# Performance work log

Hardware: AMD Instinct MI355X
Metric: run time of the kernel (lower is better)

## Reference

```python
import jax, jax.numpy as jnp
import numpy as np

B, S, D = 2, 2048, 768
C = 8                # num_channels
R = D // C           # ternary_rank = 96 (RoPE head_dim)
THETA = 10000.0
TERNARY_STD = 0.2
TERNARY_SCALE = 1.0  # ternary_factor_scaling


def _rope_tables():
    # HF-style RoPE: inv_freq over half dim, emb = concat(freqs, freqs)
    inv_freq = 1.0 / (THETA ** (np.arange(0, R, 2, dtype=np.float32) / R))
    pos = np.arange(S, dtype=np.float32)
    freqs = pos[:, None] * inv_freq[None, :]          # [S, R/2]
    emb = np.concatenate([freqs, freqs], axis=-1)     # [S, R]
    cos = np.broadcast_to(np.cos(emb)[None], (B, S, R)).copy()
    sin = np.broadcast_to(np.sin(emb)[None], (B, S, R)).copy()
    return jnp.asarray(cos), jnp.asarray(sin)


def setup_inputs() -> dict:
    key = jax.random.key(0)
    k1, k2, k3 = jax.random.split(key, 3)
    qz = jax.random.normal(k1, (B, S, D), dtype=jnp.float32)
    U = jax.random.normal(k2, (D, D), dtype=jnp.float32) * TERNARY_STD
    V = jax.random.normal(k3, (D, D), dtype=jnp.float32) * TERNARY_STD
    cos, sin = _rope_tables()
    return {"qz": qz, "cos": cos, "sin": sin, "U": U, "V": V}


def _rotate_half(x):
    h = x.shape[-1] // 2
    return jnp.concatenate([-x[..., h:], x[..., :h]], axis=-1)


def reference(qz, cos, sin, U, V):
    # cos/sin: [B,S,R] -> broadcast over channel dim -> [B,1,S,R]
    cosb = cos[:, None, :, :]
    sinb = sin[:, None, :, :]
    rope = lambda x: x * cosb + _rotate_half(x) * sinb       # apply
    rope_o = lambda x: x * cosb - _rotate_half(x) * sinb     # apply_o (inverse)

    # projections: F.linear(qz, W) == qz @ W.T
    qz_u = (qz @ U.T * TERNARY_SCALE).reshape(B, S, C, R).transpose(0, 2, 1, 3)
    qz_v = (qz @ V.T * TERNARY_SCALE).reshape(B, S, C, R).transpose(0, 2, 1, 3)

    qz_uo = rope_o(qz_u)
    qz_ur = rope(qz_u)
    qz_vr = rope(qz_v)

    # message_F: [B,C,S,S]
    message_F = jnp.einsum('bcqr,bckr->bcqk', qz_ur, qz_vr)
    # softmax(message_F / regularize_h) with regularize_h = 1/D  ->  * D
    qh = jax.nn.softmax((message_F * jnp.float32(D)).astype(jnp.float32), axis=-1).astype(qz_ur.dtype)

    qh_v1 = rope_o(jnp.einsum('bcqk,bckr->bcqr', qh, qz_vr))  # qh @ qz_v
    qh_v2 = rope(jnp.einsum('bckq,bckr->bcqr', qh, qz_uo))    # qh^T @ qz_uo

    qh_v1 = qh_v1.transpose(0, 2, 1, 3).reshape(B, S, D)
    qh_v2 = qh_v2.transpose(0, 2, 1, 3).reshape(B, S, D)

    message_G = (qh_v1 @ U + qh_v2 @ V) * TERNARY_SCALE
    return message_G
```

## Files before the change

kernel.cpp:

```cpp
#include <hip/hip_runtime.h>

typedef _Float16 f16;
typedef _Float16 f16x8 __attribute__((ext_vector_type(8)));
typedef _Float16 f16x4 __attribute__((ext_vector_type(4)));
typedef float f32x4 __attribute__((ext_vector_type(4)));

#define MFMA16(A,B,C) __builtin_amdgcn_mfma_f32_16x16x32_f16(A,B,C,0,0,0)
#define INV2048 4.8828125e-4f
#define HN (16ll*2048*96)
#define UVN 589824
#define ZC1 1107.98979f
#define ZC2 0.54101064f

__device__ __forceinline__ void split_f16(float x, f16& h, f16& l) {
    h = (f16)x;
    l = (f16)((x - (float)h) * 2048.0f);
}

__global__ __launch_bounds__(256) void k0_split(const float* __restrict__ qz,
                                                const float* __restrict__ U,
                                                const float* __restrict__ V,
                                                f16* __restrict__ qzh, f16* __restrict__ qzl,
                                                f16* __restrict__ Uh, f16* __restrict__ Ul,
                                                f16* __restrict__ Vh, f16* __restrict__ Vl) {
    const int i4 = blockIdx.x * 256 + threadIdx.x;
    {
        float4 x = *(const float4*)(qz + (size_t)i4 * 4);
        f16 h0, l0, h1, l1, h2, l2, h3, l3;
        split_f16(x.x, h0, l0); split_f16(x.y, h1, l1);
        split_f16(x.z, h2, l2); split_f16(x.w, h3, l3);
        f16x4 hv = {h0, h1, h2, h3};
        f16x4 lv = {l0, l1, l2, l3};
        *(f16x4*)(qzh + (size_t)i4 * 4) = hv;
        *(f16x4*)(qzl + (size_t)i4 * 4) = lv;
    }
    if (i4 < UVN / 4) {
        float4 x = *(const float4*)(U + (size_t)i4 * 4);
        f16 h0, l0, h1, l1, h2, l2, h3, l3;
        split_f16(x.x, h0, l0); split_f16(x.y, h1, l1);
        split_f16(x.z, h2, l2); split_f16(x.w, h3, l3);
        f16x4 hv = {h0, h1, h2, h3};
        f16x4 lv = {l0, l1, l2, l3};
        *(f16x4*)(Uh + (size_t)i4 * 4) = hv;
        *(f16x4*)(Ul + (size_t)i4 * 4) = lv;
        float4 y = *(const float4*)(V + (size_t)i4 * 4);
        split_f16(y.x, h0, l0); split_f16(y.y, h1, l1);
        split_f16(y.z, h2, l2); split_f16(y.w, h3, l3);
        f16x4 hv2 = {h0, h1, h2, h3};
        f16x4 lv2 = {l0, l1, l2, l3};
        *(f16x4*)(Vh + (size_t)i4 * 4) = hv2;
        *(f16x4*)(Vl + (size_t)i4 * 4) = lv2;
    }
}

__global__ __launch_bounds__(256, 2) void k1_proj(const f16* __restrict__ qzh,
                                                  const f16* __restrict__ qzl,
                                                  const f16* __restrict__ Uh,
                                                  const f16* __restrict__ Ul,
                                                  const f16* __restrict__ Vh,
                                                  const f16* __restrict__ Vl,
                                                  const float* __restrict__ cosb,
                                                  const float* __restrict__ sinb,
                                                  f16* __restrict__ uhp, f16* __restrict__ ulp,
                                                  f16* __restrict__ vhp, f16* __restrict__ vlp,
                                                  f16* __restrict__ vT, f16* __restrict__ oT) {
    __shared__ __align__(16) f16 smem[36864];
    f16* sAh  = smem;
    f16* sAl  = smem + 4608;
    f16* sBuh = smem + 9216;
    f16* sBul = smem + 9216 + 6912;
    f16* sBvh = smem + 9216 + 2 * 6912;
    f16* sBvl = smem + 9216 + 3 * 6912;

    const int tid = threadIdx.x;
    const int w = tid >> 6, lane = tid & 63;
    const int quad = lane >> 4, l15 = lane & 15;
    const int wr = w >> 1, wc = w & 1;
    const int bs0 = blockIdx.x * 64;
    const int c = blockIdx.y;

    const f16* Ug_h = Uh + (size_t)c * 96 * 768;
    const f16* Ug_l = Ul + (size_t)c * 96 * 768;
    const f16* Vg_h = Vh + (size_t)c * 96 * 768;
    const f16* Vg_l = Vl + (size_t)c * 96 * 768;

    f32x4 aUS[2][3] = {}, aUX[2][3] = {};
    f32x4 aVS[2][3] = {}, aVX[2][3] = {};

    for (int k0 = 0; k0 < 768; k0 += 64) {
        __syncthreads();
#pragma unroll
        for (int m = 0; m < 2; ++m) {
            int f = tid + 256 * m, row = f >> 3, cg = f & 7;
            const size_t go = (size_t)(bs0 + row) * 768 + k0 + cg * 8;
            const int lo = row * 72 + cg * 8;
            *(float4*)&sAh[lo] = *(const float4*)(qzh + go);
            *(float4*)&sAl[lo] = *(const float4*)(qzl + go);
        }
#pragma unroll
        for (int m = 0; m < 3; ++m) {
            int f = tid + 256 * m, row = f >> 3, cg = f & 7;
            const size_t go = (size_t)row * 768 + k0 + cg * 8;
            const int lo = row * 72 + cg * 8;
            *(float4*)&sBuh[lo] = *(const float4*)(Ug_h + go);
            *(float4*)&sBul[lo] = *(const float4*)(Ug_l + go);
            *(float4*)&sBvh[lo] = *(const float4*)(Vg_h + go);
            *(float4*)&sBvl[lo] = *(const float4*)(Vg_l + go);
        }
        __syncthreads();
#pragma unroll
        for (int cc = 0; cc < 2; ++cc) {
            f16x8 ah[2], al[2];
#pragma unroll
            for (int mt = 0; mt < 2; ++mt) {
                const int ar = (32 * wr + 16 * mt + l15) * 72 + cc * 32 + quad * 8;
                ah[mt] = *(const f16x8*)&sAh[ar];
                al[mt] = *(const f16x8*)&sAl[ar];
            }
#pragma unroll
            for (int nt = 0; nt < 3; ++nt) {
                const int br = (48 * wc + 16 * nt + l15) * 72 + cc * 32 + quad * 8;
                f16x8 buh = *(const f16x8*)&sBuh[br];
                f16x8 bul = *(const f16x8*)&sBul[br];
                f16x8 bvh = *(const f16x8*)&sBvh[br];
                f16x8 bvl = *(const f16x8*)&sBvl[br];
#pragma unroll
                for (int mt = 0; mt < 2; ++mt) {
                    aUS[mt][nt] = MFMA16(ah[mt], buh, aUS[mt][nt]);
                    aUX[mt][nt] = MFMA16(ah[mt], bul, aUX[mt][nt]);
                    aUX[mt][nt] = MFMA16(al[mt], buh, aUX[mt][nt]);
                    aVS[mt][nt] = MFMA16(ah[mt], bvh, aVS[mt][nt]);
                    aVX[mt][nt] = MFMA16(ah[mt], bvl, aVX[mt][nt]);
// ... 15 lines not shown
                const int sl = 32 * wr + 16 * mt + 4 * quad + r;
                const int col = 48 * wc + 16 * nt + l15;
                LU[sl * 100 + col] = aUS[mt][nt][r] + aUX[mt][nt][r] * INV2048;
                LV[sl * 100 + col] = aVS[mt][nt][r] + aVX[mt][nt][r] * INV2048;
            }
    __syncthreads();

    const int b = bs0 >> 11;
    const int s0 = bs0 & 2047;
    const int head = b * 8 + c;
    const size_t nb = (size_t)head * 2048 * 96;
    const size_t tb = (size_t)head * 96 * 2048;
    const int ty = tid >> 4, tx = tid & 15;

#pragma unroll
    for (int jj = 0; jj < 3; ++jj) {
        int r = tx + 16 * jj;
        f16 vt1[4], vt2[4], ot1[4], ot2[4];
#pragma unroll
        for (int ii = 0; ii < 4; ++ii) {
            int sl = 4 * ty + ii;
            int s = s0 + sl;
            int cbi = (b * 2048 + s) * 96 + r;
            float cc = cosb[cbi], ss = sinb[cbi];
            size_t rowb = nb + (size_t)s * 96;
            float u1 = LU[sl * 100 + r], u2 = LU[sl * 100 + r + 48];
            float v1 = LV[sl * 100 + r], v2 = LV[sl * 100 + r + 48];
            float ur1 = u1 * cc - u2 * ss, ur2 = u2 * cc + u1 * ss;
            float uo1 = u1 * cc + u2 * ss, uo2 = u2 * cc - u1 * ss;
            float vr1 = v1 * cc - v2 * ss, vr2 = v2 * cc + v1 * ss;
            f16 h, l;
            split_f16(ur1, h, l); uhp[rowb + r] = h;      ulp[rowb + r] = l;
            split_f16(ur2, h, l); uhp[rowb + r + 48] = h; ulp[rowb + r + 48] = l;
            split_f16(vr1, h, l); vhp[rowb + r] = h;      vlp[rowb + r] = l;      vt1[ii] = h;
            split_f16(vr2, h, l); vhp[rowb + r + 48] = h; vlp[rowb + r + 48] = l; vt2[ii] = h;
            ot1[ii] = (f16)uo1; ot2[ii] = (f16)uo2;
        }
        f16x4 pv1 = {vt1[0], vt1[1], vt1[2], vt1[3]};
        f16x4 pv2 = {vt2[0], vt2[1], vt2[2], vt2[3]};
        f16x4 po1 = {ot1[0], ot1[1], ot1[2], ot1[3]};
        f16x4 po2 = {ot2[0], ot2[1], ot2[2], ot2[3]};
        *(f16x4*)&vT[tb + (size_t)r * 2048 + s0 + 4 * ty] = pv1;
        *(f16x4*)&vT[tb + (size_t)(r + 48) * 2048 + s0 + 4 * ty] = pv2;
        *(f16x4*)&oT[tb + (size_t)r * 2048 + s0 + 4 * ty] = po1;
        *(f16x4*)&oT[tb + (size_t)(r + 48) * 2048 + s0 + 4 * ty] = po2;
    }
}

__global__ __launch_bounds__(256, 2) void k2_stats(const f16* __restrict__ uhp,
                                                   const f16* __restrict__ ulp,
                                                   const f16* __restrict__ vhp,
                                                   const f16* __restrict__ vlp,
                                                   float* __restrict__ Mo) {
    __shared__ f16 Bh[64 * 104];
    __shared__ f16 Bl[64 * 104];
    __shared__ float Mbuf[4][64];
    const int tid = threadIdx.x, w = tid >> 6, lane = tid & 63;
    const int quad = lane >> 4, l15 = lane & 15;
    const int q0 = blockIdx.x * 64, head = blockIdx.y;
    const f16* Ah_g = uhp + (size_t)head * 2048 * 96;
    const f16* Al_g = ulp + (size_t)head * 2048 * 96;
    const f16* Bh_g = vhp + (size_t)head * 2048 * 96;
    const f16* Bl_g = vlp + (size_t)head * 2048 * 96;

    f16x8 Afh[4][3], Afl[4][3];
#pragma unroll
    for (int mt = 0; mt < 4; ++mt)
#pragma unroll
        for (int cc = 0; cc < 3; ++cc) {
            size_t off = (size_t)(q0 + 16 * mt + l15) * 96 + cc * 32 + quad * 8;
            Afh[mt][cc] = *(const f16x8*)(Ah_g + off);
            Afl[mt][cc] = *(const f16x8*)(Al_g + off);
        }

    float m_run[4][4];
#pragma unroll
    for (int mt = 0; mt < 4; ++mt)
#pragma unroll
        for (int r = 0; r < 4; ++r) m_run[mt][r] = -3.0e38f;

    for (int k0 = 0; k0 < 2048; k0 += 64) {
        __syncthreads();
#pragma unroll
        for (int m = 0; m < 3; ++m) {
            int f = tid + 256 * m;
            int row = f / 12, c12 = f % 12;
            *(float4*)&Bh[row * 104 + c12 * 8] =
                *(const float4*)(Bh_g + (size_t)(k0 + row) * 96 + c12 * 8);
            *(float4*)&Bl[row * 104 + c12 * 8] =
                *(const float4*)(Bl_g + (size_t)(k0 + row) * 96 + c12 * 8);
        }
        __syncthreads();
        f32x4 accS[4] = {}, accX[4] = {};
#pragma unroll
        for (int cc = 0; cc < 3; ++cc) {
            f16x8 bh = *(const f16x8*)&Bh[(w * 16 + l15) * 104 + cc * 32 + quad * 8];
            f16x8 bl = *(const f16x8*)&Bl[(w * 16 + l15) * 104 + cc * 32 + quad * 8];
#pragma unroll
            for (int mt = 0; mt < 4; ++mt) {
                accS[mt] = MFMA16(Afh[mt][cc], bh, accS[mt]);
                accX[mt] = MFMA16(Afh[mt][cc], bl, accX[mt]);
                accX[mt] = MFMA16(Afl[mt][cc], bh, accX[mt]);
            }
        }
#pragma unroll
        for (int mt = 0; mt < 4; ++mt)
#pragma unroll
            for (int r = 0; r < 4; ++r) {
                float zl = fmaf(ZC1, accS[mt][r], ZC2 * accX[mt][r]);
                m_run[mt][r] = fmaxf(m_run[mt][r], zl);
            }
    }
#pragma unroll
    for (int mt = 0; mt < 4; ++mt)
#pragma unroll
        for (int r = 0; r < 4; ++r) {
            float m = m_run[mt][r];
            m = fmaxf(m, __shfl_xor(m, 1)); m = fmaxf(m, __shfl_xor(m, 2));
            m = fmaxf(m, __shfl_xor(m, 4)); m = fmaxf(m, __shfl_xor(m, 8));
            m_run[mt][r] = m;
        }
    if (l15 == 0) {
#pragma unroll
        for (int mt = 0; mt < 4; ++mt)
#pragma unroll
            for (int r = 0; r < 4; ++r)
                Mbuf[w][16 * mt + 4 * quad + r] = m_run[mt][r];
    }
    __syncthreads();
    if (tid < 64) {
        float M = -3.0e38f;
#pragma unroll
        for (int ww = 0; ww < 4; ++ww) M = fmaxf(M, Mbuf[ww][tid]);
        Mo[head * 2048 + q0 + tid] = M;
    }
}

__global__ __launch_bounds__(256, 2) void k3a(const f16* __restrict__ uhp,
                                              const f16* __restrict__ ulp,
                                              const f16* __restrict__ vhp,
                                              const f16* __restrict__ vlp,
                                              const f16* __restrict__ vT,
                                              const float* __restrict__ Mo,
                                              float* __restrict__ Lo,
                                              const float* __restrict__ cosb,
                                              const float* __restrict__ sinb,
                                              f16* __restrict__ w1) {
    __shared__ f16 Bh[64 * 104];
    __shared__ f16 Bl[64 * 104];
    __shared__ f16 Vt[112 * 72];
    __shared__ f16 P[64 * 72];
    const int tid = threadIdx.x, w = tid >> 6, lane = tid & 63;
    const int quad = lane >> 4, l15 = lane & 15;
    const int q0 = blockIdx.x * 64, head = blockIdx.y;
    const f16* Ah_g = uhp + (size_t)head * 2048 * 96;
    const f16* Al_g = ulp + (size_t)head * 2048 * 96;
    const f16* Bh_g = vhp + (size_t)head * 2048 * 96;
    const f16* Bl_g = vlp + (size_t)head * 2048 * 96;
    const f16* Vt_g = vT + (size_t)head * 96 * 2048;

    f16x8 Afh[4][3], Afl[4][3];
#pragma unroll
    for (int mt = 0; mt < 4; ++mt)
#pragma unroll
        for (int cc = 0; cc < 3; ++cc) {
            size_t off = (size_t)(q0 + 16 * mt + l15) * 96 + cc * 32 + quad * 8;
            Afh[mt][cc] = *(const f16x8*)(Ah_g + off);
            Afl[mt][cc] = *(const f16x8*)(Al_g + off);
        }
    float negM[4][4];
#pragma unroll
    for (int mt = 0; mt < 4; ++mt)
#pragma unroll
        for (int r = 0; r < 4; ++r)
            negM[mt][r] = -Mo[head * 2048 + q0 + 16 * mt + 4 * quad + r];

    if (tid < 144) {
        f16x8 ones = {(f16)1, (f16)1, (f16)1, (f16)1,
                      (f16)1, (f16)1, (f16)1, (f16)1};
        *(f16x8*)&Vt[96 * 72 + tid * 8] = ones;
    }

    f32x4 accO[7] = {};

    for (int k0 = 0; k0 < 2048; k0 += 64) {
        __syncthreads();
#pragma unroll
        for (int m = 0; m < 3; ++m) {
            int f = tid + 256 * m;
            int row = f / 12, c12 = f % 12;
            *(float4*)&Bh[row * 104 + c12 * 8] =
                *(const float4*)(Bh_g + (size_t)(k0 + row) * 96 + c12 * 8);
            *(float4*)&Bl[row * 104 + c12 * 8] =
                *(const float4*)(Bl_g + (size_t)(k0 + row) * 96 + c12 * 8);
        }
#pragma unroll
        for (int m = 0; m < 3; ++m) {
            int f = tid + 256 * m;
            int row = f >> 3, c8 = f & 7;
            *(float4*)&Vt[row * 72 + c8 * 8] =
                *(const float4*)(Vt_g + (size_t)row * 2048 + k0 + c8 * 8);
        }
        __syncthreads();
        f32x4 accS[4] = {}, accX[4] = {};
#pragma unroll
        for (int cc = 0; cc < 3; ++cc) {
            f16x8 bh = *(const f16x8*)&Bh[(w * 16 + l15) * 104 + cc * 32 + quad * 8];
            f16x8 bl = *(const f16x8*)&Bl[(w * 16 + l15) * 104 + cc * 32 + quad * 8];
#pragma unroll
            for (int mt = 0; mt < 4; ++mt) {
                accS[mt] = MFMA16(Afh[mt][cc], bh, accS[mt]);
                accX[mt] = MFMA16(Afh[mt][cc], bl, accX[mt]);
                accX[mt] = MFMA16(Afl[mt][cc], bh, accX[mt]);
            }
        }
#pragma unroll
        for (int mt = 0; mt < 4; ++mt)
#pragma unroll
            for (int r = 0; r < 4; ++r) {
                float zl = fmaf(ZC1, accS[mt][r], ZC2 * accX[mt][r]);
                P[(16 * mt + 4 * quad + r) * 72 + w * 16 + l15] =
                    (f16)exp2f(zl + negM[mt][r]);
            }
        __syncthreads();
#pragma unroll
        for (int kc = 0; kc < 2; ++kc) {
            f16x8 ap = *(const f16x8*)&P[(w * 16 + l15) * 72 + kc * 32 + quad * 8];
#pragma unroll
            for (int nt = 0; nt < 7; ++nt) {
                f16x8 bv = *(const f16x8*)&Vt[(nt * 16 + l15) * 72 + kc * 32 + quad * 8];
                accO[nt] = MFMA16(ap, bv, accO[nt]);
            }
        }
        __syncthreads();
    }
    float invL[4];
#pragma unroll
    for (int r = 0; r < 4; ++r) invL[r] = 1.0f / accO[6][r];
    if (l15 == 0) {
#pragma unroll
        for (int r = 0; r < 4; ++r)
            Lo[head * 2048 + q0 + w * 16 + quad * 4 + r] = accO[6][r];
    }

    const int b = head >> 3, c = head & 7;
#pragma unroll
    for (int r = 0; r < 4; ++r) {
        int q = q0 + w * 16 + quad * 4 + r;
        int cbi = (b * 2048 + q) * 96;
        f16* wrow = w1 + (size_t)(b * 2048 + q) * 768 + c * 96;
#pragma unroll
        for (int nt = 0; nt < 3; ++nt) {
            int rr = nt * 16 + l15;
            float cc = cosb[cbi + rr], ss = sinb[cbi + rr];
            float a = accO[nt][r] * invL[r];
            float b2 = accO[nt + 3][r] * invL[r];
            wrow[rr] = (f16)(a * cc + b2 * ss);
            wrow[rr + 48] = (f16)(b2 * cc - a * ss);
        }
    }
}

__global__ __launch_bounds__(256, 2) void k3b(const f16* __restrict__ uhp,
                                              const f16* __restrict__ ulp,
                                              const f16* __restrict__ vhp,
                                              const f16* __restrict__ vlp,
                                              const f16* __restrict__ oT,
                                              const float* __restrict__ Mo,
                                              const float* __restrict__ Lo,
                                              const float* __restrict__ cosb,
                                              const float* __restrict__ sinb,
                                              f16* __restrict__ w2) {
    __shared__ f16 Bh[64 * 104];
    __shared__ f16 Bl[64 * 104];
    __shared__ f16 Ot[96 * 72];
    __shared__ f16 P[64 * 72];
    const int tid = threadIdx.x, w = tid >> 6, lane = tid & 63;
    const int quad = lane >> 4, l15 = lane & 15;
    const int q0 = blockIdx.x * 64, head = blockIdx.y;
    const f16* Ah_g = vhp + (size_t)head * 2048 * 96;
    const f16* Al_g = vlp + (size_t)head * 2048 * 96;
    const f16* Bh_g = uhp + (size_t)head * 2048 * 96;
    const f16* Bl_g = ulp + (size_t)head * 2048 * 96;
    const f16* Ot_g = oT + (size_t)head * 96 * 2048;

    f16x8 Afh[4][3], Afl[4][3];
#pragma unroll
    for (int mt = 0; mt < 4; ++mt)
#pragma unroll
        for (int cc = 0; cc < 3; ++cc) {
            size_t off = (size_t)(q0 + 16 * mt + l15) * 96 + cc * 32 + quad * 8;
            Afh[mt][cc] = *(const f16x8*)(Ah_g + off);
            Afl[mt][cc] = *(const f16x8*)(Al_g + off);
        }

    f32x4 accO[6] = {};

    for (int k0 = 0; k0 < 2048; k0 += 64) {
        float negMk = -Mo[head * 2048 + k0 + w * 16 + l15];
        float invLk = 1.0f / Lo[head * 2048 + k0 + w * 16 + l15];
        __syncthreads();
#pragma unroll
        for (int m = 0; m < 3; ++m) {
            int f = tid + 256 * m;
            int row = f / 12, c12 = f % 12;
            *(float4*)&Bh[row * 104 + c12 * 8] =
                *(const float4*)(Bh_g + (size_t)(k0 + row) * 96 + c12 * 8);
            *(float4*)&Bl[row * 104 + c12 * 8] =
                *(const float4*)(Bl_g + (size_t)(k0 + row) * 96 + c12 * 8);
        }
#pragma unroll
        for (int m = 0; m < 3; ++m) {
            int f = tid + 256 * m;
            int row = f >> 3, c8 = f & 7;
            *(float4*)&Ot[row * 72 + c8 * 8] =
                *(const float4*)(Ot_g + (size_t)row * 2048 + k0 + c8 * 8);
        }
        __syncthreads();
        f32x4 accS[4] = {}, accX[4] = {};
#pragma unroll
        for (int cc = 0; cc < 3; ++cc) {
            f16x8 bh = *(const f16x8*)&Bh[(w * 16 + l15) * 104 + cc * 32 + quad * 8];
            f16x8 bl = *(const f16x8*)&Bl[(w * 16 + l15) * 104 + cc * 32 + quad * 8];
#pragma unroll
            for (int mt = 0; mt < 4; ++mt) {
                accS[mt] = MFMA16(Afh[mt][cc], bh, accS[mt]);
                accX[mt] = MFMA16(Afl[mt][cc], bh, accX[mt]);
                accX[mt] = MFMA16(Afh[mt][cc], bl, accX[mt]);
            }
        }
#pragma unroll
        for (int mt = 0; mt < 4; ++mt)
#pragma unroll
            for (int r = 0; r < 4; ++r) {
                float zl = fmaf(ZC1, accS[mt][r], ZC2 * accX[mt][r]);
                P[(16 * mt + 4 * quad + r) * 72 + w * 16 + l15] =
                    (f16)(exp2f(zl + negMk) * invLk);
            }
        __syncthreads();
#pragma unroll
        for (int kc = 0; kc < 2; ++kc) {
            f16x8 ap = *(const f16x8*)&P[(w * 16 + l15) * 72 + kc * 32 + quad * 8];
#pragma unroll
            for (int nt = 0; nt < 6; ++nt) {
                f16x8 bo = *(const f16x8*)&Ot[(nt * 16 + l15) * 72 + kc * 32 + quad * 8];
                accO[nt] = MFMA16(ap, bo, accO[nt]);
            }
        }
        __syncthreads();
    }
    const int b = head >> 3, c = head & 7;
#pragma unroll
    for (int r = 0; r < 4; ++r) {
        int q = q0 + w * 16 + quad * 4 + r;
        int cbi = (b * 2048 + q) * 96;
        f16* wrow = w2 + (size_t)(b * 2048 + q) * 768 + c * 96;
#pragma unroll
        for (int nt = 0; nt < 3; ++nt) {
            int rr = nt * 16 + l15;
            float cc = cosb[cbi + rr], ss = sinb[cbi + rr];
            float a = accO[nt][r];
            float b2 = accO[nt + 3][r];
            wrow[rr] = (f16)(a * cc - b2 * ss);
            wrow[rr + 48] = (f16)(b2 * cc + a * ss);
        }
    }
}

__global__ __launch_bounds__(256, 2) void k4_final(const f16* __restrict__ w1,
                                                   const f16* __restrict__ w2,
                                                   const float* __restrict__ U,
                                                   const float* __restrict__ V,
                                                   float* __restrict__ outp) {
    __shared__ f16 A1[128 * 56];
    __shared__ f16 A2[128 * 56];
    __shared__ f16 B1[64 * 56];
    __shared__ f16 B2[64 * 56];
    const int tid = threadIdx.x, w = tid >> 6, lane = tid & 63;
    const int quad = lane >> 4, l15 = lane & 15;
    const int bs0 = blockIdx.x * 128;
    const int d0 = blockIdx.y * 64;
    f32x4 acc[2][4] = {};

    for (int ec = 0; ec < 24; ++ec) {
        int e0 = ec * 32;
        __syncthreads();
#pragma unroll
        for (int m = 0; m < 2; ++m) {
            int f = tid + 256 * m;
            int row = f >> 2, q = f & 3;
            *(float4*)&A1[row * 56 + q * 8] =
                *(const float4*)(w1 + (size_t)(bs0 + row) * 768 + e0 + q * 8);
            *(float4*)&A2[row * 56 + q * 8] =
                *(const float4*)(w2 + (size_t)(bs0 + row) * 768 + e0 + q * 8);
        }
#pragma unroll
        for (int m2 = 0; m2 < 2; ++m2) {
            int e_r = (tid >> 4) + 16 * m2;
            int dc = tid & 15;
            float4 fu = *(const float4*)(U + (size_t)(e0 + e_r) * 768 + d0 + dc * 4);
            float4 fv = *(const float4*)(V + (size_t)(e0 + e_r) * 768 + d0 + dc * 4);
            B1[(dc * 4 + 0) * 56 + e_r] = (f16)fu.x;
// ... 77 lines not shown
```

Measured before the change: 339.8 us.

## Prefetch next K tile into registers and double-buffer shared tiles in attention kernels

The stats, k3a and k3b kernels now issue global loads for the next 64-row K/V tile into registers before computing on the current tile, then write them to shared memory after the score MFMAs. Vt/Ot (and Bh/Bl in k2_stats) are double-buffered so the store does not race with readers, and one barrier per iteration is removed in k2. This aims to hide global load latency behind MFMA work, at the cost of extra LDS and registers, which may reduce occupancy under launch_bounds(256,2).

```diff
diff --git a/kernel.cpp b/kernel.cpp
--- a/kernel.cpp
+++ b/kernel.cpp
@@ -199,8 +199,8 @@
                                                    const f16* __restrict__ vhp,
                                                    const f16* __restrict__ vlp,
                                                    float* __restrict__ Mo) {
-    __shared__ f16 Bh[64 * 104];
-    __shared__ f16 Bl[64 * 104];
+    __shared__ f16 Bh[2][64 * 104];
+    __shared__ f16 Bl[2][64 * 104];
     __shared__ float Mbuf[4][64];
     const int tid = threadIdx.x, w = tid >> 6, lane = tid & 63;
     const int quad = lane >> 4, l15 = lane & 15;
@@ -220,29 +220,49 @@
             Afl[mt][cc] = *(const f16x8*)(Al_g + off);
         }
 
+    const int sr0 = tid / 12,         sc0 = (tid % 12) * 8;
+    const int sr1 = (tid + 256) / 12, sc1 = ((tid + 256) % 12) * 8;
+    const int sr2 = (tid + 512) / 12, sc2 = ((tid + 512) % 12) * 8;
+
+    float4 h0, h1, h2, g0, g1, g2;
+
     float m_run[4][4];
 #pragma unroll
     for (int mt = 0; mt < 4; ++mt)
 #pragma unroll
         for (int r = 0; r < 4; ++r) m_run[mt][r] = -3.0e38f;
 
-    for (int k0 = 0; k0 < 2048; k0 += 64) {
-        __syncthreads();
-#pragma unroll
-        for (int m = 0; m < 3; ++m) {
-            int f = tid + 256 * m;
-            int row = f / 12, c12 = f % 12;
-            *(float4*)&Bh[row * 104 + c12 * 8] =
-                *(const float4*)(Bh_g + (size_t)(k0 + row) * 96 + c12 * 8);
-            *(float4*)&Bl[row * 104 + c12 * 8] =
-                *(const float4*)(Bl_g + (size_t)(k0 + row) * 96 + c12 * 8);
-        }
-        __syncthreads();
+    h0 = *(const float4*)(Bh_g + (size_t)sr0 * 96 + sc0);
+    h1 = *(const float4*)(Bh_g + (size_t)sr1 * 96 + sc1);
+    h2 = *(const float4*)(Bh_g + (size_t)sr2 * 96 + sc2);
+    g0 = *(const float4*)(Bl_g + (size_t)sr0 * 96 + sc0);
+    g1 = *(const float4*)(Bl_g + (size_t)sr1 * 96 + sc1);
+    g2 = *(const float4*)(Bl_g + (size_t)sr2 * 96 + sc2);
+    *(float4*)&Bh[0][sr0 * 104 + sc0] = h0;
+    *(float4*)&Bh[0][sr1 * 104 + sc1] = h1;
+    *(float4*)&Bh[0][sr2 * 104 + sc2] = h2;
+    *(float4*)&Bl[0][sr0 * 104 + sc0] = g0;
+    *(float4*)&Bl[0][sr1 * 104 + sc1] = g1;
+    *(float4*)&Bl[0][sr2 * 104 + sc2] = g2;
+    __syncthreads();
+
+    for (int t = 0; t < 32; ++t) {
+        const int cur = t & 1;
+        if (t < 31) {
+            const f16* bg = Bh_g + (size_t)(t + 1) * 6144;
+            const f16* lg = Bl_g + (size_t)(t + 1) * 6144;
+            h0 = *(const float4*)(bg + (size_t)sr0 * 96 + sc0);
+            h1 = *(const float4*)(bg + (size_t)sr1 * 96 + sc1);
+            h2 = *(const float4*)(bg + (size_t)sr2 * 96 + sc2);
+            g0 = *(const float4*)(lg + (size_t)sr0 * 96 + sc0);
+            g1 = *(const float4*)(lg + (size_t)sr1 * 96 + sc1);
+            g2 = *(const float4*)(lg + (size_t)sr2 * 96 + sc2);
+        }
         f32x4 accS[4] = {}, accX[4] = {};
 #pragma unroll
         for (int cc = 0; cc < 3; ++cc) {
-            f16x8 bh = *(const f16x8*)&Bh[(w * 16 + l15) * 104 + cc * 32 + quad * 8];
-            f16x8 bl = *(const f16x8*)&Bl[(w * 16 + l15) * 104 + cc * 32 + quad * 8];
+            f16x8 bh = *(const f16x8*)&Bh[cur][(w * 16 + l15) * 104 + cc * 32 + quad * 8];
+            f16x8 bl = *(const f16x8*)&Bl[cur][(w * 16 + l15) * 104 + cc * 32 + quad * 8];
 #pragma unroll
             for (int mt = 0; mt < 4; ++mt) {
                 accS[mt] = MFMA16(Afh[mt][cc], bh, accS[mt]);
@@ -257,6 +277,15 @@
                 float zl = fmaf(ZC1, accS[mt][r], ZC2 * accX[mt][r]);
                 m_run[mt][r] = fmaxf(m_run[mt][r], zl);
             }
+        if (t < 31) {
+            *(float4*)&Bh[cur ^ 1][sr0 * 104 + sc0] = h0;
+            *(float4*)&Bh[cur ^ 1][sr1 * 104 + sc1] = h1;
+            *(float4*)&Bh[cur ^ 1][sr2 * 104 + sc2] = h2;
+            *(float4*)&Bl[cur ^ 1][sr0 * 104 + sc0] = g0;
+            *(float4*)&Bl[cur ^ 1][sr1 * 104 + sc1] = g1;
+            *(float4*)&Bl[cur ^ 1][sr2 * 104 + sc2] = g2;
+        }
+        __syncthreads();
     }
 #pragma unroll
     for (int mt = 0; mt < 4; ++mt)
@@ -295,7 +324,7 @@
                                               f16* __restrict__ w1) {
     __shared__ f16 Bh[64 * 104];
     __shared__ f16 Bl[64 * 104];
-    __shared__ f16 Vt[112 * 72];
+    __shared__ f16 Vt[2][112 * 72];
     __shared__ f16 P[64 * 72];
     const int tid = threadIdx.x, w = tid >> 6, lane = tid & 63;
     const int quad = lane >> 4, l15 = lane & 15;
@@ -322,33 +351,58 @@
         for (int r = 0; r < 4; ++r)
             negM[mt][r] = -Mo[head * 2048 + q0 + 16 * mt + 4 * quad + r];
 
+    const int sr0 = tid / 12,         sc0 = (tid % 12) * 8;
+    const int sr1 = (tid + 256) / 12, sc1 = ((tid + 256) % 12) * 8;
+    const int sr2 = (tid + 512) / 12, sc2 = ((tid + 512) % 12) * 8;
+    const int vr0 = tid >> 3, vcc = (tid & 7) * 8;
+
+    float4 h0, h1, h2, g0, g1, g2, v0, v1, v2;
+
     if (tid < 144) {
         f16x8 ones = {(f16)1, (f16)1, (f16)1, (f16)1,
                       (f16)1, (f16)1, (f16)1, (f16)1};
-        *(f16x8*)&Vt[96 * 72 + tid * 8] = ones;
-    }
+        *(f16x8*)&Vt[0][96 * 72 + tid * 8] = ones;
+        *(f16x8*)&Vt[1][96 * 72 + tid * 8] = ones;
+    }
+
+    h0 = *(const float4*)(Bh_g + (size_t)sr0 * 96 + sc0);
+    h1 = *(const float4*)(Bh_g + (size_t)sr1 * 96 + sc1);
+    h2 = *(const float4*)(Bh_g + (size_t)sr2 * 96 + sc2);
+    g0 = *(const float4*)(Bl_g + (size_t)sr0 * 96 + sc0);
+    g1 = *(const float4*)(Bl_g + (size_t)sr1 * 96 + sc1);
+    g2 = *(const float4*)(Bl_g + (size_t)sr2 * 96 + sc2);
+    v0 = *(const float4*)(Vt_g + (size_t)vr0 * 2048 + vcc);
+    v1 = *(const float4*)(Vt_g + (size_t)(vr0 + 32) * 2048 + vcc);
+    v2 = *(const float4*)(Vt_g + (size_t)(vr0 + 64) * 2048 + vcc);
+    *(float4*)&Bh[sr0 * 104 + sc0] = h0;
+    *(float4*)&Bh[sr1 * 104 + sc1] = h1;
+    *(float4*)&Bh[sr2 * 104 + sc2] = h2;
+    *(float4*)&Bl[sr0 * 104 + sc0] = g0;
+    *(float4*)&Bl[sr1 * 104 + sc1] = g1;
+    *(float4*)&Bl[sr2 * 104 + sc2] = g2;
+    *(float4*)&Vt[0][vr0 * 72 + vcc] = v0;
+    *(float4*)&Vt[0][(vr0 + 32) * 72 + vcc] = v1;
+    *(float4*)&Vt[0][(vr0 + 64) * 72 + vcc] = v2;
+    __syncthreads();
 
     f32x4 accO[7] = {};
-
-    for (int k0 = 0; k0 < 2048; k0 += 64) {
-        __syncthreads();
-#pragma unroll
-        for (int m = 0; m < 3; ++m) {
-            int f = tid + 256 * m;
-            int row = f / 12, c12 = f % 12;
-            *(float4*)&Bh[row * 104 + c12 * 8] =
-                *(const float4*)(Bh_g + (size_t)(k0 + row) * 96 + c12 * 8);
-            *(float4*)&Bl[row * 104 + c12 * 8] =
-                *(const float4*)(Bl_g + (size_t)(k0 + row) * 96 + c12 * 8);
-        }
-#pragma unroll
-        for (int m = 0; m < 3; ++m) {
-            int f = tid + 256 * m;
-            int row = f >> 3, c8 = f & 7;
-            *(float4*)&Vt[row * 72 + c8 * 8] =
-                *(const float4*)(Vt_g + (size_t)row * 2048 + k0 + c8 * 8);
-        }
-        __syncthreads();
+    int pcur = 0;
+
+    for (int t = 0; t < 32; ++t) {
+        if (t < 31) {
+            const f16* bg = Bh_g + (size_t)(t + 1) * 6144;
+            const f16* lg = Bl_g + (size_t)(t + 1) * 6144;
+            const int kn = (t + 1) * 64;
+            h0 = *(const float4*)(bg + (size_t)sr0 * 96 + sc0);
+            h1 = *(const float4*)(bg + (size_t)sr1 * 96 + sc1);
+            h2 = *(const float4*)(bg + (size_t)sr2 * 96 + sc2);
+            g0 = *(const float4*)(lg + (size_t)sr0 * 96 + sc0);
+            g1 = *(const float4*)(lg + (size_t)sr1 * 96 + sc1);
+            g2 = *(const float4*)(lg + (size_t)sr2 * 96 + sc2);
+            v0 = *(const float4*)(Vt_g + (size_t)vr0 * 2048 + kn + vcc);
+            v1 = *(const float4*)(Vt_g + (size_t)(vr0 + 32) * 2048 + kn + vcc);
+            v2 = *(const float4*)(Vt_g + (size_t)(vr0 + 64) * 2048 + kn + vcc);
+        }
         f32x4 accS[4] = {}, accX[4] = {};
 #pragma unroll
         for (int cc = 0; cc < 3; ++cc) {
@@ -370,16 +424,28 @@
                     (f16)exp2f(zl + negM[mt][r]);
             }
         __syncthreads();
+        if (t < 31) {
+            *(float4*)&Bh[sr0 * 104 + sc0] = h0;
+            *(float4*)&Bh[sr1 * 104 + sc1] = h1;
+            *(float4*)&Bh[sr2 * 104 + sc2] = h2;
+            *(float4*)&Bl[sr0 * 104 + sc0] = g0;
+            *(float4*)&Bl[sr1 * 104 + sc1] = g1;
+            *(float4*)&Bl[sr2 * 104 + sc2] = g2;
+            *(float4*)&Vt[pcur ^ 1][vr0 * 72 + vcc] = v0;
+            *(float4*)&Vt[pcur ^ 1][(vr0 + 32) * 72 + vcc] = v1;
+            *(float4*)&Vt[pcur ^ 1][(vr0 + 64) * 72 + vcc] = v2;
+        }
 #pragma unroll
         for (int kc = 0; kc < 2; ++kc) {
             f16x8 ap = *(const f16x8*)&P[(w * 16 + l15) * 72 + kc * 32 + quad * 8];
 #pragma unroll
             for (int nt = 0; nt < 7; ++nt) {
-                f16x8 bv = *(const f16x8*)&Vt[(nt * 16 + l15) * 72 + kc * 32 + quad * 8];
+                f16x8 bv = *(const f16x8*)&Vt[pcur][(nt * 16 + l15) * 72 + kc * 32 + quad * 8];
                 accO[nt] = MFMA16(ap, bv, accO[nt]);
             }
         }
         __syncthreads();
+        pcur ^= 1;
     }
     float invL[4];
 #pragma unroll
@@ -420,7 +486,7 @@
                                               f16* __restrict__ w2) {
     __shared__ f16 Bh[64 * 104];
     __shared__ f16 Bl[64 * 104];
-    __shared__ f16 Ot[96 * 72];
+    __shared__ f16 Ot[2][96 * 72];
     __shared__ f16 P[64 * 72];
     const int tid = threadIdx.x, w = tid >> 6, lane = tid & 63;
     const int quad = lane >> 4, l15 = lane & 15;
@@ -441,29 +507,54 @@
             Afl[mt][cc] = *(const f16x8*)(Al_g + off);
         }
 
+    const int sr0 = tid / 12,         sc0 = (tid % 12) * 8;
+    const int sr1 = (tid + 256) / 12, sc1 = ((tid + 256) % 12) * 8;
+    const int sr2 = (tid + 512) / 12, sc2 = ((tid + 512) % 12) * 8;
+    const int vr0 = tid >> 3, vcc = (tid & 7) * 8;
+
+    float4 h0, h1, h2, g0, g1, g2, v0, v1, v2;
+
+    h0 = *(const float4*)(Bh_g + (size_t)sr0 * 96 + sc0);
+    h1 = *(const float4*)(Bh_g + (size_t)sr1 * 96 + sc1);
+    h2 = *(const float4*)(Bh_g + (size_t)sr2 * 96 + sc2);
+    g0 = *(const float4*)(Bl_g + (size_t)sr0 * 96 + sc0);
+    g1 = *(const float4*)(Bl_g + (size_t)sr1 * 96 + sc1);
+    g2 = *(const float4*)(Bl_g + (size_t)sr2 * 96 + sc2);
+    v0 = *(const float4*)(Ot_g + (size_t)vr0 * 2048 + vcc);
+    v1 = *(const float4*)(Ot_g + (size_t)(vr0 + 32) * 2048 + vcc);
+    v2 = *(const float4*)(Ot_g + (size_t)(vr0 + 64) * 2048 + vcc);
+    *(float4*)&Bh[sr0 * 104 + sc0] = h0;
+    *(float4*)&Bh[sr1 * 104 + sc1] = h1;
+    *(float4*)&Bh[sr2 * 104 + sc2] = h2;
+    *(float4*)&Bl[sr0 * 104 + sc0] = g0;
+    *(float4*)&Bl[sr1 * 104 + sc1] = g1;
+    *(float4*)&Bl[sr2 * 104 + sc2] = g2;
+    *(float4*)&Ot[0][vr0 * 72 + vcc] = v0;
+    *(float4*)&Ot[0][(vr0 + 32) * 72 + vcc] = v1;
+    *(float4*)&Ot[0][(vr0 + 64) * 72 + vcc] = v2;
+    __syncthreads();
+
     f32x4 accO[6] = {};
-
-    for (int k0 = 0; k0 < 2048; k0 += 64) {
+    int pcur = 0;
+
+    for (int t = 0; t < 32; ++t) {
+        const int k0 = t * 64;
         float negMk = -Mo[head * 2048 + k0 + w * 16 + l15];
         float invLk = 1.0f / Lo[head * 2048 + k0 + w * 16 + l15];
-        __syncthreads();
-#pragma unroll
-        for (int m = 0; m < 3; ++m) {
-            int f = tid + 256 * m;
-            int row = f / 12, c12 = f % 12;
-            *(float4*)&Bh[row * 104 + c12 * 8] =
-                *(const float4*)(Bh_g + (size_t)(k0 + row) * 96 + c12 * 8);
-            *(float4*)&Bl[row * 104 + c12 * 8] =
-                *(const float4*)(Bl_g + (size_t)(k0 + row) * 96 + c12 * 8);
-        }
-#pragma unroll
-        for (int m = 0; m < 3; ++m) {
-            int f = tid + 256 * m;
-            int row = f >> 3, c8 = f & 7;
-            *(float4*)&Ot[row * 72 + c8 * 8] =
-                *(const float4*)(Ot_g + (size_t)row * 2048 + k0 + c8 * 8);
-        }
-        __syncthreads();
+        if (t < 31) {
+            const f16* bg = Bh_g + (size_t)(t + 1) * 6144;
+            const f16* lg = Bl_g + (size_t)(t + 1) * 6144;
+            const int kn = (t + 1) * 64;
+            h0 = *(const float4*)(bg + (size_t)sr0 * 96 + sc0);
+            h1 = *(const float4*)(bg + (size_t)sr1 * 96 + sc1);
+            h2 = *(const float4*)(bg + (size_t)sr2 * 96 + sc2);
+            g0 = *(const float4*)(lg + (size_t)sr0 * 96 + sc0);
+            g1 = *(const float4*)(lg + (size_t)sr1 * 96 + sc1);
+            g2 = *(const float4*)(lg + (size_t)sr2 * 96 + sc2);
+            v0 = *(const float4*)(Ot_g + (size_t)vr0 * 2048 + kn + vcc);
+            v1 = *(const float4*)(Ot_g + (size_t)(vr0 + 32) * 2048 + kn + vcc);
+            v2 = *(const float4*)(Ot_g + (size_t)(vr0 + 64) * 2048 + kn + vcc);
+        }
         f32x4 accS[4] = {}, accX[4] = {};
 #pragma unroll
         for (int cc = 0; cc < 3; ++cc) {
@@ -485,16 +576,28 @@
                     (f16)(exp2f(zl + negMk) * invLk);
             }
         __syncthreads();
+        if (t < 31) {
+            *(float4*)&Bh[sr0 * 104 + sc0] = h0;
+            *(float4*)&Bh[sr1 * 104 + sc1] = h1;
+            *(float4*)&Bh[sr2 * 104 + sc2] = h2;
+            *(float4*)&Bl[sr0 * 104 + sc0] = g0;
+            *(float4*)&Bl[sr1 * 104 + sc1] = g1;
+            *(float4*)&Bl[sr2 * 104 + sc2] = g2;
+            *(float4*)&Ot[pcur ^ 1][vr0 * 72 + vcc] = v0;
+            *(float4*)&Ot[pcur ^ 1][(vr0 + 32) * 72 + vcc] = v1;
+            *(float4*)&Ot[pcur ^ 1][(vr0 + 64) * 72 + vcc] = v2;
+        }
 #pragma unroll
         for (int kc = 0; kc < 2; ++kc) {
             f16x8 ap = *(const f16x8*)&P[(w * 16 + l15) * 72 + kc * 32 + quad * 8];
 #pragma unroll
             for (int nt = 0; nt < 6; ++nt) {
-                f16x8 bo = *(const f16x8*)&Ot[(nt * 16 + l15) * 72 + kc * 32 + quad * 8];
+                f16x8 bo = *(const f16x8*)&Ot[pcur][(nt * 16 + l15) * 72 + kc * 32 + quad * 8];
                 accO[nt] = MFMA16(ap, bo, accO[nt]);
             }
         }
         __syncthreads();
+        pcur ^= 1;
     }
     const int b = head >> 3, c = head & 7;
 #pragma unroll
```

After: 334.3 us. Within noise of the previous version (-1.6%).

## Pipeline attention kernels with register-prefetched K tiles and double-buffered LDS

Applied to the files above, without the earlier changes.

The stats and both attention-apply kernels stop staging the K operand (split-f16 hi/lo) through shared memory. Each wave now loads its own K fragments directly into registers, prefetching the next tile while the current one is computed. The V/O transposed tiles and the P buffer are double-buffered in LDS, which removes two of the three barriers per iteration. The kernels also use s_setprio around MFMA blocks, an XOR-style column swizzle for P to reduce bank conflicts, and a block-index swizzle that groups neighbouring blocks for L2 reuse. In exchange, register pressure and shared-memory footprint go up, which could lower occupancy, and the single remaining barrier per tile must still order the P and Vt writes correctly.

```diff
diff --git a/kernel.cpp b/kernel.cpp
--- a/kernel.cpp
+++ b/kernel.cpp
@@ -76,8 +76,10 @@
     const int w = tid >> 6, lane = tid & 63;
     const int quad = lane >> 4, l15 = lane & 15;
     const int wr = w >> 1, wc = w & 1;
-    const int bs0 = blockIdx.x * 64;
-    const int c = blockIdx.y;
+    const int bid0 = blockIdx.y * 64 + blockIdx.x;
+    const int swz  = (bid0 & 7) * 64 + (bid0 >> 3);
+    const int bs0 = (swz & 63) * 64;
+    const int c = swz >> 6;
 
     const f16* Ug_h = Uh + (size_t)c * 96 * 768;
     const f16* Ug_l = Ul + (size_t)c * 96 * 768;
@@ -199,16 +201,14 @@
                                                    const f16* __restrict__ vhp,
                                                    const f16* __restrict__ vlp,
                                                    float* __restrict__ Mo) {
-    __shared__ f16 Bh[64 * 104];
-    __shared__ f16 Bl[64 * 104];
     __shared__ float Mbuf[4][64];
     const int tid = threadIdx.x, w = tid >> 6, lane = tid & 63;
     const int quad = lane >> 4, l15 = lane & 15;
-    const int q0 = blockIdx.x * 64, head = blockIdx.y;
+    const int bid0 = blockIdx.y * 32 + blockIdx.x;
+    const int swz  = (bid0 & 7) * 64 + (bid0 >> 3);
+    const int q0 = (swz & 31) * 64, head = swz >> 5;
     const f16* Ah_g = uhp + (size_t)head * 2048 * 96;
     const f16* Al_g = ulp + (size_t)head * 2048 * 96;
-    const f16* Bh_g = vhp + (size_t)head * 2048 * 96;
-    const f16* Bl_g = vlp + (size_t)head * 2048 * 96;
 
     f16x8 Afh[4][3], Afl[4][3];
 #pragma unroll
@@ -220,43 +220,54 @@
             Afl[mt][cc] = *(const f16x8*)(Al_g + off);
         }
 
+    const f16* Bh_p = vhp + (size_t)head * 2048 * 96 + (size_t)(w * 16 + l15) * 96 + quad * 8;
+    const f16* Bl_p = vlp + (size_t)head * 2048 * 96 + (size_t)(w * 16 + l15) * 96 + quad * 8;
+
+    f16x8 Bch[2][3], Bcl[2][3];
+#pragma unroll
+    for (int cc = 0; cc < 3; ++cc) {
+        Bch[0][cc] = *(const f16x8*)(Bh_p + cc * 32);
+        Bcl[0][cc] = *(const f16x8*)(Bl_p + cc * 32);
+    }
+
     float m_run[4][4];
 #pragma unroll
     for (int mt = 0; mt < 4; ++mt)
 #pragma unroll
         for (int r = 0; r < 4; ++r) m_run[mt][r] = -3.0e38f;
 
-    for (int k0 = 0; k0 < 2048; k0 += 64) {
-        __syncthreads();
-#pragma unroll
-        for (int m = 0; m < 3; ++m) {
-            int f = tid + 256 * m;
-            int row = f / 12, c12 = f % 12;
-            *(float4*)&Bh[row * 104 + c12 * 8] =
-                *(const float4*)(Bh_g + (size_t)(k0 + row) * 96 + c12 * 8);
-            *(float4*)&Bl[row * 104 + c12 * 8] =
-                *(const float4*)(Bl_g + (size_t)(k0 + row) * 96 + c12 * 8);
-        }
-        __syncthreads();
-        f32x4 accS[4] = {}, accX[4] = {};
-#pragma unroll
-        for (int cc = 0; cc < 3; ++cc) {
-            f16x8 bh = *(const f16x8*)&Bh[(w * 16 + l15) * 104 + cc * 32 + quad * 8];
-            f16x8 bl = *(const f16x8*)&Bl[(w * 16 + l15) * 104 + cc * 32 + quad * 8];
-#pragma unroll
-            for (int mt = 0; mt < 4; ++mt) {
-                accS[mt] = MFMA16(Afh[mt][cc], bh, accS[mt]);
-                accX[mt] = MFMA16(Afh[mt][cc], bl, accX[mt]);
-                accX[mt] = MFMA16(Afl[mt][cc], bh, accX[mt]);
-            }
-        }
-#pragma unroll
-        for (int mt = 0; mt < 4; ++mt)
-#pragma unroll
-            for (int r = 0; r < 4; ++r) {
-                float zl = fmaf(ZC1, accS[mt][r], ZC2 * accX[mt][r]);
-                m_run[mt][r] = fmaxf(m_run[mt][r], zl);
-            }
+    for (int tp = 0; tp < 16; ++tp) {
+#pragma unroll
+        for (int h = 0; h < 2; ++h) {
+            const int t = 2 * tp + h;
+            if (t < 31) {
+                const f16* bh = Bh_p + (size_t)(t + 1) * 6144;
+                const f16* bl = Bl_p + (size_t)(t + 1) * 6144;
+#pragma unroll
+                for (int cc = 0; cc < 3; ++cc) {
+                    Bch[h ^ 1][cc] = *(const f16x8*)(bh + cc * 32);
+                    Bcl[h ^ 1][cc] = *(const f16x8*)(bl + cc * 32);
+                }
+            }
+            f32x4 accS[4] = {}, accX[4] = {};
+            __builtin_amdgcn_s_setprio(1);
+#pragma unroll
+            for (int cc = 0; cc < 3; ++cc)
+#pragma unroll
+                for (int mt = 0; mt < 4; ++mt) {
+                    accS[mt] = MFMA16(Afh[mt][cc], Bch[h][cc], accS[mt]);
+                    accX[mt] = MFMA16(Afh[mt][cc], Bcl[h][cc], accX[mt]);
+                    accX[mt] = MFMA16(Afl[mt][cc], Bch[h][cc], accX[mt]);
+                }
+            __builtin_amdgcn_s_setprio(0);
+#pragma unroll
+            for (int mt = 0; mt < 4; ++mt)
+#pragma unroll
+                for (int r = 0; r < 4; ++r) {
+                    float zl = fmaf(ZC1, accS[mt][r], ZC2 * accX[mt][r]);
+                    m_run[mt][r] = fmaxf(m_run[mt][r], zl);
+                }
+        }
     }
 #pragma unroll
     for (int mt = 0; mt < 4; ++mt)
@@ -293,17 +304,15 @@
                                               const float* __restrict__ cosb,
                                               const float* __restrict__ sinb,
                                               f16* __restrict__ w1) {
-    __shared__ f16 Bh[64 * 104];
-    __shared__ f16 Bl[64 * 104];
-    __shared__ f16 Vt[112 * 72];
-    __shared__ f16 P[64 * 72];
+    __shared__ f16 Vt[2][112 * 72];
+    __shared__ f16 P[2][64 * 72];
     const int tid = threadIdx.x, w = tid >> 6, lane = tid & 63;
     const int quad = lane >> 4, l15 = lane & 15;
-    const int q0 = blockIdx.x * 64, head = blockIdx.y;
+    const int bid0 = blockIdx.y * 32 + blockIdx.x;
+    const int swz  = (bid0 & 7) * 64 + (bid0 >> 3);
+    const int q0 = (swz & 31) * 64, head = swz >> 5;
     const f16* Ah_g = uhp + (size_t)head * 2048 * 96;
     const f16* Al_g = ulp + (size_t)head * 2048 * 96;
-    const f16* Bh_g = vhp + (size_t)head * 2048 * 96;
-    const f16* Bl_g = vlp + (size_t)head * 2048 * 96;
     const f16* Vt_g = vT + (size_t)head * 96 * 2048;
 
     f16x8 Afh[4][3], Afl[4][3];
@@ -322,64 +331,90 @@
         for (int r = 0; r < 4; ++r)
             negM[mt][r] = -Mo[head * 2048 + q0 + 16 * mt + 4 * quad + r];
 
+    const f16* Bh_p = vhp + (size_t)head * 2048 * 96 + (size_t)(w * 16 + l15) * 96 + quad * 8;
+    const f16* Bl_p = vlp + (size_t)head * 2048 * 96 + (size_t)(w * 16 + l15) * 96 + quad * 8;
+    const int vr0 = tid >> 3, vc8 = (tid & 7) * 8;
+    const int pwc = (w * 16 + l15 + 16 * quad) & 63;
+    const int prr = 16 * (l15 >> 2);
+
     if (tid < 144) {
         f16x8 ones = {(f16)1, (f16)1, (f16)1, (f16)1,
                       (f16)1, (f16)1, (f16)1, (f16)1};
-        *(f16x8*)&Vt[96 * 72 + tid * 8] = ones;
-    }
+        *(f16x8*)&Vt[0][96 * 72 + tid * 8] = ones;
+        *(f16x8*)&Vt[1][96 * 72 + tid * 8] = ones;
+    }
+
+    f16x8 Bch[2][3], Bcl[2][3];
+    float4 v0, v1, v2;
+#pragma unroll
+    for (int cc = 0; cc < 3; ++cc) {
+        Bch[0][cc] = *(const f16x8*)(Bh_p + cc * 32);
+        Bcl[0][cc] = *(const f16x8*)(Bl_p + cc * 32);
+    }
+    v0 = *(const float4*)(Vt_g + (size_t)vr0 * 2048 + vc8);
+    v1 = *(const float4*)(Vt_g + (size_t)(vr0 + 32) * 2048 + vc8);
+    v2 = *(const float4*)(Vt_g + (size_t)(vr0 + 64) * 2048 + vc8);
+    *(float4*)&Vt[0][vr0 * 72 + vc8] = v0;
+    *(float4*)&Vt[0][(vr0 + 32) * 72 + vc8] = v1;
+    *(float4*)&Vt[0][(vr0 + 64) * 72 + vc8] = v2;
 
     f32x4 accO[7] = {};
 
-    for (int k0 = 0; k0 < 2048; k0 += 64) {
-        __syncthreads();
-#pragma unroll
-        for (int m = 0; m < 3; ++m) {
-            int f = tid + 256 * m;
-            int row = f / 12, c12 = f % 12;
-            *(float4*)&Bh[row * 104 + c12 * 8] =
-                *(const float4*)(Bh_g + (size_t)(k0 + row) * 96 + c12 * 8);
-            *(float4*)&Bl[row * 104 + c12 * 8] =
-                *(const float4*)(Bl_g + (size_t)(k0 + row) * 96 + c12 * 8);
-        }
-#pragma unroll
-        for (int m = 0; m < 3; ++m) {
-            int f = tid + 256 * m;
-            int row = f >> 3, c8 = f & 7;
-            *(float4*)&Vt[row * 72 + c8 * 8] =
-                *(const float4*)(Vt_g + (size_t)row * 2048 + k0 + c8 * 8);
-        }
-        __syncthreads();
-        f32x4 accS[4] = {}, accX[4] = {};
-#pragma unroll
-        for (int cc = 0; cc < 3; ++cc) {
-            f16x8 bh = *(const f16x8*)&Bh[(w * 16 + l15) * 104 + cc * 32 + quad * 8];
-            f16x8 bl = *(const f16x8*)&Bl[(w * 16 + l15) * 104 + cc * 32 + quad * 8];
-#pragma unroll
-            for (int mt = 0; mt < 4; ++mt) {
-                accS[mt] = MFMA16(Afh[mt][cc], bh, accS[mt]);
-                accX[mt] = MFMA16(Afh[mt][cc], bl, accX[mt]);
-                accX[mt] = MFMA16(Afl[mt][cc], bh, accX[mt]);
-            }
-        }
-#pragma unroll
-        for (int mt = 0; mt < 4; ++mt)
-#pragma unroll
-            for (int r = 0; r < 4; ++r) {
-                float zl = fmaf(ZC1, accS[mt][r], ZC2 * accX[mt][r]);
-                P[(16 * mt + 4 * quad + r) * 72 + w * 16 + l15] =
-                    (f16)exp2f(zl + negM[mt][r]);
-            }
-        __syncthreads();
-#pragma unroll
-        for (int kc = 0; kc < 2; ++kc) {
-            f16x8 ap = *(const f16x8*)&P[(w * 16 + l15) * 72 + kc * 32 + quad * 8];
-#pragma unroll
-            for (int nt = 0; nt < 7; ++nt) {
-                f16x8 bv = *(const f16x8*)&Vt[(nt * 16 + l15) * 72 + kc * 32 + quad * 8];
-                accO[nt] = MFMA16(ap, bv, accO[nt]);
-            }
-        }
-        __syncthreads();
+    for (int tp = 0; tp < 16; ++tp) {
+#pragma unroll
+        for (int h = 0; h < 2; ++h) {
+            const int t = 2 * tp + h;
+            if (t < 31) {
+                const f16* bh = Bh_p + (size_t)(t + 1) * 6144;
+                const f16* bl = Bl_p + (size_t)(t + 1) * 6144;
+                const int kn = (t + 1) * 64;
+#pragma unroll
+                for (int cc = 0; cc < 3; ++cc) {
+                    Bch[h ^ 1][cc] = *(const f16x8*)(bh + cc * 32);
+                    Bcl[h ^ 1][cc] = *(const f16x8*)(bl + cc * 32);
+                }
+                v0 = *(const float4*)(Vt_g + (size_t)vr0 * 2048 + kn + vc8);
+                v1 = *(const float4*)(Vt_g + (size_t)(vr0 + 32) * 2048 + kn + vc8);
+                v2 = *(const float4*)(Vt_g + (size_t)(vr0 + 64) * 2048 + kn + vc8);
+            }
+            f32x4 accS[4] = {}, accX[4] = {};
+            __builtin_amdgcn_s_setprio(1);
+#pragma unroll
+            for (int cc = 0; cc < 3; ++cc)
+#pragma unroll
+                for (int mt = 0; mt < 4; ++mt) {
+                    accS[mt] = MFMA16(Afh[mt][cc], Bch[h][cc], accS[mt]);
+                    accX[mt] = MFMA16(Afh[mt][cc], Bcl[h][cc], accX[mt]);
+                    accX[mt] = MFMA16(Afl[mt][cc], Bch[h][cc], accX[mt]);
+                }
+            __builtin_amdgcn_s_setprio(0);
+#pragma unroll
+            for (int mt = 0; mt < 4; ++mt)
+#pragma unroll
+                for (int r = 0; r < 4; ++r) {
+                    float zl = fmaf(ZC1, accS[mt][r], ZC2 * accX[mt][r]);
+                    P[h][(16 * mt + 4 * quad + r) * 72 + pwc] =
+                        (f16)exp2f(zl + negM[mt][r]);
+                }
+            __syncthreads();
+            __builtin_amdgcn_s_setprio(1);
+#pragma unroll
+            for (int kc = 0; kc < 2; ++kc) {
+                f16x8 ap = *(const f16x8*)&P[h][(w * 16 + l15) * 72 +
+                                               ((kc * 32 + quad * 8 + prr) & 63)];
+#pragma unroll
+                for (int nt = 0; nt < 7; ++nt) {
+                    f16x8 bv = *(const f16x8*)&Vt[h][(nt * 16 + l15) * 72 + kc * 32 + quad * 8];
+                    accO[nt] = MFMA16(ap, bv, accO[nt]);
+                }
+            }
+            __builtin_amdgcn_s_setprio(0);
+            if (t < 31) {
+                *(float4*)&Vt[h ^ 1][vr0 * 72 + vc8] = v0;
+                *(float4*)&Vt[h ^ 1][(vr0 + 32) * 72 + vc8] = v1;
+                *(float4*)&Vt[h ^ 1][(vr0 + 64) * 72 + vc8] = v2;
+            }
+        }
     }
     float invL[4];
 #pragma unroll
@@ -418,17 +453,15 @@
                                               const float* __restrict__ cosb,
                                               const float* __restrict__ sinb,
                                               f16* __restrict__ w2) {
-    __shared__ f16 Bh[64 * 104];
-    __shared__ f16 Bl[64 * 104];
-    __shared__ f16 Ot[96 * 72];
-    __shared__ f16 P[64 * 72];
+    __shared__ f16 Ot[2][96 * 72];
+    __shared__ f16 P[2][64 * 72];
     const int tid = threadIdx.x, w = tid >> 6, lane = tid & 63;
     const int quad = lane >> 4, l15 = lane & 15;
-    const int q0 = blockIdx.x * 64, head = blockIdx.y;
+    const int bid0 = blockIdx.y * 32 + blockIdx.x;
+    const int swz  = (bid0 & 7) * 64 + (bid0 >> 3);
+    const int q0 = (swz & 31) * 64, head = swz >> 5;
     const f16* Ah_g = vhp + (size_t)head * 2048 * 96;
     const f16* Al_g = vlp + (size_t)head * 2048 * 96;
-    const f16* Bh_g = uhp + (size_t)head * 2048 * 96;
-    const f16* Bl_g = ulp + (size_t)head * 2048 * 96;
     const f16* Ot_g = oT + (size_t)head * 96 * 2048;
 
     f16x8 Afh[4][3], Afl[4][3];
@@ -441,60 +474,86 @@
             Afl[mt][cc] = *(const f16x8*)(Al_g + off);
         }
 
+    const f16* Bh_p = uhp + (size_t)head * 2048 * 96 + (size_t)(w * 16 + l15) * 96 + quad * 8;
+    const f16* Bl_p = ulp + (size_t)head * 2048 * 96 + (size_t)(w * 16 + l15) * 96 + quad * 8;
+    const int vr0 = tid >> 3, vc8 = (tid & 7) * 8;
+    const int pwc = (w * 16 + l15 + 16 * quad) & 63;
+    const int prr = 16 * (l15 >> 2);
+
+    f16x8 Bch[2][3], Bcl[2][3];
+    float4 v0, v1, v2;
+#pragma unroll
+    for (int cc = 0; cc < 3; ++cc) {
+        Bch[0][cc] = *(const f16x8*)(Bh_p + cc * 32);
+        Bcl[0][cc] = *(const f16x8*)(Bl_p + cc * 32);
+    }
+    v0 = *(const float4*)(Ot_g + (size_t)vr0 * 2048 + vc8);
+    v1 = *(const float4*)(Ot_g + (size_t)(vr0 + 32) * 2048 + vc8);
+    v2 = *(const float4*)(Ot_g + (size_t)(vr0 + 64) * 2048 + vc8);
+    *(float4*)&Ot[0][vr0 * 72 + vc8] = v0;
+    *(float4*)&Ot[0][(vr0 + 32) * 72 + vc8] = v1;
+    *(float4*)&Ot[0][(vr0 + 64) * 72 + vc8] = v2;
+
     f32x4 accO[6] = {};
 
-    for (int k0 = 0; k0 < 2048; k0 += 64) {
-        float negMk = -Mo[head * 2048 + k0 + w * 16 + l15];
-        float invLk = 1.0f / Lo[head * 2048 + k0 + w * 16 + l15];
-        __syncthreads();
-#pragma unroll
-        for (int m = 0; m < 3; ++m) {
-            int f = tid + 256 * m;
-            int row = f / 12, c12 = f % 12;
-            *(float4*)&Bh[row * 104 + c12 * 8] =
-                *(const float4*)(Bh_g + (size_t)(k0 + row) * 96 + c12 * 8);
-            *(float4*)&Bl[row * 104 + c12 * 8] =
-                *(const float4*)(Bl_g + (size_t)(k0 + row) * 96 + c12 * 8);
-        }
-#pragma unroll
-        for (int m = 0; m < 3; ++m) {
-            int f = tid + 256 * m;
-            int row = f >> 3, c8 = f & 7;
-            *(float4*)&Ot[row * 72 + c8 * 8] =
-                *(const float4*)(Ot_g + (size_t)row * 2048 + k0 + c8 * 8);
-        }
-        __syncthreads();
-        f32x4 accS[4] = {}, accX[4] = {};
-#pragma unroll
-        for (int cc = 0; cc < 3; ++cc) {
-            f16x8 bh = *(const f16x8*)&Bh[(w * 16 + l15) * 104 + cc * 32 + quad * 8];
-            f16x8 bl = *(const f16x8*)&Bl[(w * 16 + l15) * 104 + cc * 32 + quad * 8];
-#pragma unroll
-            for (int mt = 0; mt < 4; ++mt) {
-                accS[mt] = MFMA16(Afh[mt][cc], bh, accS[mt]);
-                accX[mt] = MFMA16(Afl[mt][cc], bh, accX[mt]);
-                accX[mt] = MFMA16(Afh[mt][cc], bl, accX[mt]);
-            }
-        }
-#pragma unroll
-        for (int mt = 0; mt < 4; ++mt)
-#pragma unroll
-            for (int r = 0; r < 4; ++r) {
-                float zl = fmaf(ZC1, accS[mt][r], ZC2 * accX[mt][r]);
-                P[(16 * mt + 4 * quad + r) * 72 + w * 16 + l15] =
-                    (f16)(exp2f(zl + negMk) * invLk);
-            }
-        __syncthreads();
-#pragma unroll
-        for (int kc = 0; kc < 2; ++kc) {
-            f16x8 ap = *(const f16x8*)&P[(w * 16 + l15) * 72 + kc * 32 + quad * 8];
-#pragma unroll
-            for (int nt = 0; nt < 6; ++nt) {
-                f16x8 bo = *(const f16x8*)&Ot[(nt * 16 + l15) * 72 + kc * 32 + quad * 8];
-                accO[nt] = MFMA16(ap, bo, accO[nt]);
-            }
-        }
-        __syncthreads();
+    for (int tp = 0; tp < 16; ++tp) {
+#pragma unroll
+        for (int h = 0; h < 2; ++h) {
+            const int t = 2 * tp + h;
+            const int k0 = t * 64;
+            float negMk = -Mo[head * 2048 + k0 + w * 16 + l15];
+            float invLk = 1.0f / Lo[head * 2048 + k0 + w * 16 + l15];
+            if (t < 31) {
+                const f16* bh = Bh_p + (size_t)(t + 1) * 6144;
+                const f16* bl = Bl_p + (size_t)(t + 1) * 6144;
+                const int kn = (t + 1) * 64;
+#pragma unroll
+                for (int cc = 0; cc < 3; ++cc) {
+                    Bch[h ^ 1][cc] = *(const f16x8*)(bh + cc * 32);
+                    Bcl[h ^ 1][cc] = *(const f16x8*)(bl + cc * 32);
+                }
+                v0 = *(const float4*)(Ot_g + (size_t)vr0 * 2048 + kn + vc8);
+                v1 = *(const float4*)(Ot_g + (size_t)(vr0 + 32) * 2048 + kn + vc8);
+                v2 = *(const float4*)(Ot_g + (size_t)(vr0 + 64) * 2048 + kn + vc8);
+            }
+            f32x4 accS[4] = {}, accX[4] = {};
+            __builtin_amdgcn_s_setprio(1);
+#pragma unroll
+            for (int cc = 0; cc < 3; ++cc)
+#pragma unroll
+                for (int mt = 0; mt < 4; ++mt) {
+                    accS[mt] = MFMA16(Afh[mt][cc], Bch[h][cc], accS[mt]);
+                    accX[mt] = MFMA16(Afl[mt][cc], Bch[h][cc], accX[mt]);
+                    accX[mt] = MFMA16(Afh[mt][cc], Bcl[h][cc], accX[mt]);
+                }
+            __builtin_amdgcn_s_setprio(0);
+#pragma unroll
+            for (int mt = 0; mt < 4; ++mt)
+#pragma unroll
+                for (int r = 0; r < 4; ++r) {
+                    float zl = fmaf(ZC1, accS[mt][r], ZC2 * accX[mt][r]);
+                    P[h][(16 * mt + 4 * quad + r) * 72 + pwc] =
+                        (f16)(exp2f(zl + negMk) * invLk);
+                }
+            __syncthreads();
+            __builtin_amdgcn_s_setprio(1);
+#pragma unroll
+            for (int kc = 0; kc < 2; ++kc) {
+                f16x8 ap = *(const f16x8*)&P[h][(w * 16 + l15) * 72 +
+                                               ((kc * 32 + quad * 8 + prr) & 63)];
+#pragma unroll
+                for (int nt = 0; nt < 6; ++nt) {
+                    f16x8 bo = *(const f16x8*)&Ot[h][(nt * 16 + l15) * 72 + kc * 32 + quad * 8];
+                    accO[nt] = MFMA16(ap, bo, accO[nt]);
+                }
+            }
+            __builtin_amdgcn_s_setprio(0);
+            if (t < 31) {
+                *(float4*)&Ot[h ^ 1][vr0 * 72 + vc8] = v0;
+                *(float4*)&Ot[h ^ 1][(vr0 + 32) * 72 + vc8] = v1;
+                *(float4*)&Ot[h ^ 1][(vr0 + 64) * 72 + vc8] = v2;
+            }
+        }
     }
     const int b = head >> 3, c = head & 7;
 #pragma unroll
```

After: 326.3 us. 1.04x faster.
